# Optimization experiments

Hardware: AMD Instinct MI355X
Metric: run time of the kernel (lower is better)

The kernel has to match this reference:

```python
import jax, jax.numpy as jnp
import numpy as np

USER_NUM = 100000
ITEM_NUM = 50000
N_NODES = USER_NUM + ITEM_NUM
EMB_DIM = 64
N_LAYERS = 3
NNZ = 4800000


def setup_inputs() -> dict:
    key = jax.random.key(0)
    k1, k2, k3, k4, k5 = jax.random.split(key, 5)
    user_emb = 0.2 * jax.random.normal(k1, (USER_NUM, EMB_DIM), dtype=jnp.float32)
    item_emb = 0.2 * jax.random.normal(k2, (ITEM_NUM, EMB_DIM), dtype=jnp.float32)
    adj_row = jax.random.randint(k3, (NNZ,), 0, N_NODES, dtype=jnp.int32)
    adj_col = jax.random.randint(k4, (NNZ,), 0, N_NODES, dtype=jnp.int32)
    adj_vals = jax.random.uniform(k5, (NNZ,), dtype=jnp.float32)
    return {
        "user_emb": user_emb,
        "item_emb": item_emb,
        "adj_row": adj_row,
        "adj_col": adj_col,
        "adj_vals": adj_vals,
    }


def _spmm(row, col, vals, x):
    # sparse [N,N] @ dense [N,D] via gather + weighted segment-sum
    msg = vals[:, None] * x[col]  # [nnz, D]
    return jax.ops.segment_sum(msg, row, num_segments=N_NODES)


def reference(user_emb, item_emb, adj_row, adj_col, adj_vals):
    ego = jnp.concatenate([user_emb, item_emb], axis=0)  # [N, D]
    acc = ego  # running sum over layers (equivalent to stack+mean)
    for _ in range(N_LAYERS):
        ego = _spmm(adj_row, adj_col, adj_vals, ego)
        acc = acc + ego
    out = acc / jnp.asarray(N_LAYERS + 1, dtype=acc.dtype)
    return out[:USER_NUM], out[USER_NUM:]
```

## Files before the change

### kernel.cpp

```cpp
#include <hip/hip_runtime.h>

#define USER_NUM 100000
#define ITEM_NUM 50000
#define N_NODES  150000
#define EMB_DIM  64
#define NNZ      4800000

#define CB_SHIFT 10
#define ROWS_PER_CB 1024
#define NCB ((N_NODES + ROWS_PER_CB - 1) / ROWS_PER_CB)
#define CB_CAP 34000
#define TILE 2048
#define NTILES ((NNZ + TILE - 1) / TILE)
#define EPT 8
#define CUR_STRIDE 16

__device__ __forceinline__ float bflo(unsigned u) {
    return __uint_as_float(u << 16);
}
__device__ __forceinline__ float bfhi(unsigned u) {
    return __uint_as_float(u & 0xFFFF0000u);
}
__device__ __forceinline__ unsigned f2bf(float f) {
    unsigned u = __float_as_uint(f);
    return (u + 0x7FFFu + ((u >> 16) & 1u)) >> 16;
}

__global__ void lgcn_init(const float4* __restrict__ user,
                          const float4* __restrict__ item,
                          uint4* __restrict__ xb,
                          int* __restrict__ bucket_cursor) {
    int i = blockIdx.x * blockDim.x + threadIdx.x;
    if (i < NCB) bucket_cursor[i * CUR_STRIDE] = i * CB_CAP;
    if (i >= N_NODES * 8) return;
    const int user_chunks = USER_NUM * 8;
    float4 f0, f1;
    if (i < user_chunks) {
        f0 = user[i * 2];
        f1 = user[i * 2 + 1];
    } else {
        f0 = item[(i - user_chunks) * 2];
        f1 = item[(i - user_chunks) * 2 + 1];
    }
    uint4 p;
    p.x = f2bf(f0.x) | (f2bf(f0.y) << 16);
    p.y = f2bf(f0.z) | (f2bf(f0.w) << 16);
    p.z = f2bf(f1.x) | (f2bf(f1.y) << 16);
    p.w = f2bf(f1.z) | (f2bf(f1.w) << 16);
    xb[i] = p;
}

__global__ __launch_bounds__(256, 8) void lgcn_partition(
    const int* __restrict__ row,
    const int* __restrict__ col,
    const float* __restrict__ vals,
    int* __restrict__ bucket_cursor,
    int2* __restrict__ t_cv) {
    __shared__ int histB[NCB];
    __shared__ int delta[NCB];
    __shared__ int2 pcv[TILE];
    __shared__ unsigned char bb[TILE];
    int* sscan = (int*)pcv;

    int tid = threadIdx.x;
    int tileStart = blockIdx.x * TILE;
    int tileCount = NNZ - tileStart;
    if (tileCount > TILE) tileCount = TILE;

    for (int b = tid; b < NCB; b += 256) histB[b] = 0;
    __syncthreads();

    int rws[EPT];
    int lps[EPT];
#pragma unroll
    for (int k = 0; k < EPT; ++k) {
        int le = tid + k * 256;
        int r = -1, lp = 0;
        if (le < tileCount) {
            r = row[tileStart + le];
            lp = atomicAdd(&histB[r >> CB_SHIFT], 1);
        }
        rws[k] = r;
        lps[k] = lp;
    }
    __syncthreads();

    int h = (tid < NCB) ? histB[tid] : 0;
    sscan[tid] = h;
    __syncthreads();
    for (int off = 1; off < 256; off <<= 1) {
        int x = (tid >= off) ? sscan[tid - off] : 0;
        __syncthreads();
        sscan[tid] += x;
        __syncthreads();
    }
    int sb = 0, rb = 0;
    if (tid < NCB) {
        sb = sscan[tid] - h;
        rb = h ? atomicAdd(&bucket_cursor[tid * CUR_STRIDE], h) : 0;
    }
    __syncthreads();
    if (tid < NCB) {
        histB[tid] = sb;
        delta[tid] = rb - sb;
    }
    __syncthreads();

#pragma unroll
    for (int k = 0; k < EPT; ++k) {
        int le = tid + k * 256;
        if (le < tileCount) {
            int e = tileStart + le;
            int cc = col[e];
            float vv = vals[e];
            int r = rws[k];
            int b = r >> CB_SHIFT;
            int slot = histB[b] + lps[k];
            pcv[slot] = make_int2(((r & (ROWS_PER_CB - 1)) << 18) | cc,
                                  __float_as_int(vv));
            bb[slot] = (unsigned char)b;
        }
    }
    __syncthreads();

#pragma unroll
    for (int k = 0; k < EPT; ++k) {
        int i = tid + k * 256;
        if (i < tileCount) {
            int b = bb[i];
            int gpos = delta[b] + i;
            if (gpos < (b + 1) * CB_CAP)
                t_cv[gpos] = pcv[i];
        }
    }
}

__global__ __launch_bounds__(1024) void lgcn_finalize(
    const int* __restrict__ bucket_cursor,
    const int2* __restrict__ t_cv,
    int2* __restrict__ csr_cv,
    int2* __restrict__ row_se) {
    __shared__ int hist[ROWS_PER_CB];
    __shared__ int cur[ROWS_PER_CB];
    __shared__ int sscan[1024];
    int t = threadIdx.x;
    int b = blockIdx.x;

    int v = 0;
    if (t < NCB) {
        int cb = bucket_cursor[t * CUR_STRIDE] - t * CB_CAP;
        v = (cb > CB_CAP) ? CB_CAP : cb;
    }
    if (t < 256) sscan[t] = v;
    __syncthreads();
    for (int off = 1; off < 256; off <<= 1) {
        int x = 0;
        if (t < 256 && t >= off) x = sscan[t - off];
        __syncthreads();
        if (t < 256) sscan[t] += x;
        __syncthreads();
    }
    int prev = (b == 0) ? 0 : sscan[b - 1];
    int bbase = prev;
    int count = sscan[b] - prev;
    __syncthreads();

    int lo = b * ROWS_PER_CB;
    int nrows = N_NODES - lo;
    if (nrows > ROWS_PER_CB) nrows = ROWS_PER_CB;

    hist[t] = 0;
    __syncthreads();

    int base = b * CB_CAP;
    int eEnd = base + count;
    int e = base + t;
    for (; e + 3 * 1024 < eEnd; e += 4 * 1024) {
        int2 c0 = t_cv[e];
        int2 c1 = t_cv[e + 1024];
        int2 c2 = t_cv[e + 2048];
        int2 c3 = t_cv[e + 3072];
        atomicAdd(&hist[(unsigned)c0.x >> 18], 1);
        atomicAdd(&hist[(unsigned)c1.x >> 18], 1);
        atomicAdd(&hist[(unsigned)c2.x >> 18], 1);
        atomicAdd(&hist[(unsigned)c3.x >> 18], 1);
    }
    for (; e < eEnd; e += 1024)
        atomicAdd(&hist[(unsigned)t_cv[e].x >> 18], 1);
    __syncthreads();

    int h = hist[t];
    sscan[t] = h;
    __syncthreads();
    for (int off = 1; off < 1024; off <<= 1) {
        int x = (t >= off) ? sscan[t - off] : 0;
        __syncthreads();
        sscan[t] += x;
        __syncthreads();
    }
    int p = bbase + sscan[t] - h;
    if (t < nrows) {
        row_se[lo + t] = make_int2(p, p + h);
        cur[t] = p;
    }
    __syncthreads();

    e = base + t;
    for (; e + 3 * 1024 < eEnd; e += 4 * 1024) {
        int2 c0 = t_cv[e];
        int2 c1 = t_cv[e + 1024];
        int2 c2 = t_cv[e + 2048];
        int2 c3 = t_cv[e + 3072];
        int p0 = atomicAdd(&cur[(unsigned)c0.x >> 18], 1);
        int p1 = atomicAdd(&cur[(unsigned)c1.x >> 18], 1);
        int p2 = atomicAdd(&cur[(unsigned)c2.x >> 18], 1);
        int p3 = atomicAdd(&cur[(unsigned)c3.x >> 18], 1);
        csr_cv[p0] = make_int2(c0.x & 0x3FFFF, c0.y);
        csr_cv[p1] = make_int2(c1.x & 0x3FFFF, c1.y);
        csr_cv[p2] = make_int2(c2.x & 0x3FFFF, c2.y);
        csr_cv[p3] = make_int2(c3.x & 0x3FFFF, c3.y);
    }
    for (; e < eEnd; e += 1024) {
        int2 cv = t_cv[e];
        int pos = atomicAdd(&cur[(unsigned)cv.x >> 18], 1);
        csr_cv[pos] = make_int2(cv.x & 0x3FFFF, cv.y);
    }
}

#define FMA8(vv, uu) do {                                          \
    a[0] += (vv) * bflo((uu).x); a[1] += (vv) * bfhi((uu).x);      \
    a[2] += (vv) * bflo((uu).y); a[3] += (vv) * bfhi((uu).y);      \
    a[4] += (vv) * bflo((uu).z); a[5] += (vv) * bfhi((uu).z);      \
    a[6] += (vv) * bflo((uu).w); a[7] += (vv) * bfhi((uu).w);      \
} while (0)

#define SPMM_BODY                                                  \
    int gid = blockIdx.x * blockDim.x + threadIdx.x;               \
    int r = gid >> 6;                                              \
    if (r >= N_NODES) return;                                      \
    int lane = threadIdx.x & 63;                                   \
    int c = lane & 7;                                              \
    int sub = lane >> 3;                                           \
    int2 se = row_se[r];                                           \
    int start = se.x;                                              \
    int end = se.y;                                                \
    float a[8] = {0.f, 0.f, 0.f, 0.f, 0.f, 0.f, 0.f, 0.f};         \
    int e = start + sub;                                           \
    for (; e + 24 < end; e += 32) {                                \
        int2 cv0 = csr_cv[e];                                      \
        int2 cv1 = csr_cv[e + 8];                                  \
        int2 cv2 = csr_cv[e + 16];                                 \
        int2 cv3 = csr_cv[e + 24];                                 \
        uint4 u0 = xb[cv0.x * 8 + c];                              \
        uint4 u1 = xb[cv1.x * 8 + c];                              \
        uint4 u2 = xb[cv2.x * 8 + c];                              \
        uint4 u3 = xb[cv3.x * 8 + c];                              \
        float v0 = __int_as_float(cv0.y);                          \
        float v1 = __int_as_float(cv1.y);                          \
        float v2 = __int_as_float(cv2.y);                          \
        float v3 = __int_as_float(cv3.y);                          \
        FMA8(v0, u0);                                              \
        FMA8(v1, u1);                                              \
        FMA8(v2, u2);                                              \
        FMA8(v3, u3);                                              \
    }                                                              \
    if (e + 8 < end) {                                             \
        int2 cv0 = csr_cv[e];                                      \
        int2 cv1 = csr_cv[e + 8];                                  \
        uint4 u0 = xb[cv0.x * 8 + c];                              \
        uint4 u1 = xb[cv1.x * 8 + c];                              \
        float v0 = __int_as_float(cv0.y);                          \
        float v1 = __int_as_float(cv1.y);                          \
        FMA8(v0, u0);                                              \
        FMA8(v1, u1);                                              \
        e += 16;                                                   \
    }                                                              \
    if (e < end) {                                                 \
        int2 cv = csr_cv[e];                                       \
        uint4 u = xb[cv.x * 8 + c];                                \
        float v = __int_as_float(cv.y);                            \
        FMA8(v, u);                                                \
    }                                                              \
    _Pragma("unroll")                                              \
    for (int k = 0; k < 8; ++k) {                                  \
        a[k] += __shfl_xor(a[k], 8);                               \
        a[k] += __shfl_xor(a[k], 16);                              \
        a[k] += __shfl_xor(a[k], 32);                              \
    }

__global__ __launch_bounds__(256, 8) void lgcn_spmm_bf16(
    const int2* __restrict__ row_se,
    const int2* __restrict__ csr_cv,
    const uint4* __restrict__ xb,
    uint4* __restrict__ yb) {
    SPMM_BODY
    if (sub == 0) {
        uint4 p;
        p.x = f2bf(a[0]) | (f2bf(a[1]) << 16);
        p.y = f2bf(a[2]) | (f2bf(a[3]) << 16);
        p.z = f2bf(a[4]) | (f2bf(a[5]) << 16);
        p.w = f2bf(a[6]) | (f2bf(a[7]) << 16);
        yb[r * 8 + c] = p;
    }
}

__global__ __launch_bounds__(256, 8) void lgcn_spmm_final(
    const int2* __restrict__ row_se,
    const int2* __restrict__ csr_cv,
    const uint4* __restrict__ xb,
    const uint4* __restrict__ x0b,
    const uint4* __restrict__ y1b,
    float4* __restrict__ out) {
    SPMM_BODY
    if (sub == 0) {
        uint4 q0 = x0b[r * 8 + c];
        uint4 q1 = y1b[r * 8 + c];
        uint4 q2 = xb[r * 8 + c];
        float4 o0, o1;
        o0.x = (bflo(q0.x) + bflo(q1.x) + bflo(q2.x) + a[0]) * 0.25f;
        o0.y = (bfhi(q0.x) + bfhi(q1.x) + bfhi(q2.x) + a[1]) * 0.25f;
        o0.z = (bflo(q0.y) + bflo(q1.y) + bflo(q2.y) + a[2]) * 0.25f;
        o0.w = (bfhi(q0.y) + bfhi(q1.y) + bfhi(q2.y) + a[3]) * 0.25f;
        o1.x = (bflo(q0.z) + bflo(q1.z) + bflo(q2.z) + a[4]) * 0.25f;
        o1.y = (bfhi(q0.z) + bfhi(q1.z) + bfhi(q2.z) + a[5]) * 0.25f;
        o1.z = (bflo(q0.w) + bflo(q1.w) + bflo(q2.w) + a[6]) * 0.25f;
        o1.w = (bfhi(q0.w) + bfhi(q1.w) + bfhi(q2.w) + a[7]) * 0.25f;
        int idx = r * 16 + c * 2;
        out[idx] = o0;
        out[idx + 1] = o1;
    }
}

extern "C" void kernel_launch(void* const* d_in, const int* in_sizes, int n_in,
                              void* d_out, int out_size, void* d_ws, size_t ws_size,
                              hipStream_t stream) {
    const float* user_emb = (const float*)d_in[0];
    const float* item_emb = (const float*)d_in[1];
    const int*   adj_row  = (const int*)d_in[2];
    const int*   adj_col  = (const int*)d_in[3];
    const float* adj_vals = (const float*)d_in[4];
    float* out = (float*)d_out;

    char* base = (char*)d_ws;
    uint4* xb_a   = (uint4*)base;
    int2*  csr_cv = (int2*)(base + 19200000);
    char*  S      = base + 57600000;
    const size_t T_ENTRIES = (size_t)NCB * CB_CAP;
    int2*  t_cv   = (int2*)S;
    uint4* y1b    = (uint4*)S;
    uint4* y2b    = (uint4*)(S + 19200000);
    char*  tail   = S + T_ENTRIES * 8;
    int2*  row_se = (int2*)tail;
    int*   bucket_cursor = (int*)(tail + (size_t)N_NODES * 8);

    {
        int threads = 256;
        int blocks = (N_NODES * 8 + threads - 1) / threads;
        lgcn_init<<<blocks, threads, 0, stream>>>(
            (const float4*)user_emb, (const float4*)item_emb, xb_a,
            bucket_cursor);
    }

    lgcn_partition<<<NTILES, 256, 0, stream>>>(
        adj_row, adj_col, adj_vals, bucket_cursor, t_cv);
    lgcn_finalize<<<NCB, 1024, 0, stream>>>(
        bucket_cursor, t_cv, csr_cv, row_se);

    const int spmm_block = 256;
    const int spmm_grid = (N_NODES * 64 + spmm_block - 1) / spmm_block;
    lgcn_spmm_bf16<<<spmm_grid, spmm_block, 0, stream>>>(
        row_se, csr_cv, xb_a, y1b);
    lgcn_spmm_bf16<<<spmm_grid, spmm_block, 0, stream>>>(
        row_se, csr_cv, y1b, y2b);
    lgcn_spmm_final<<<spmm_grid, spmm_block, 0, stream>>>(
        row_se, csr_cv, y2b, xb_a, y1b, (float4*)out);
}
```

Measured before the change: 507.9 us.

## Halve row buckets, widen partition blocks, use nontemporal loads/stores in SpMM

Row buckets shrink from 1024 to 512 rows, which doubles the bucket count to 293. The partition kernel moves to 512 threads per block so its scan covers every bucket, and the finalize scan widens to 1024 entries. The SpMM kernels switch the CSR edge stream, the layer outputs and the final output to nontemporal loads and stores, so the gathered embedding rows keep more of the cache. The trade-off is more global cursor atomics and per-block scan work during partitioning, in exchange for smaller finalize blocks and less cache pollution.

```diff
diff --git a/kernel.cpp b/kernel.cpp
--- a/kernel.cpp
+++ b/kernel.cpp
@@ -6,13 +6,14 @@
 #define EMB_DIM  64
 #define NNZ      4800000
 
-#define CB_SHIFT 10
-#define ROWS_PER_CB 1024
+#define CB_SHIFT 9
+#define ROWS_PER_CB 512
 #define NCB ((N_NODES + ROWS_PER_CB - 1) / ROWS_PER_CB)
-#define CB_CAP 34000
+#define CB_CAP 17024
 #define TILE 2048
 #define NTILES ((NNZ + TILE - 1) / TILE)
-#define EPT 8
+#define PT_THREADS 512
+#define EPT (TILE / PT_THREADS)
 #define CUR_STRIDE 16
 
 __device__ __forceinline__ float bflo(unsigned u) {
@@ -24,6 +25,27 @@
 __device__ __forceinline__ unsigned f2bf(float f) {
     unsigned u = __float_as_uint(f);
     return (u + 0x7FFFu + ((u >> 16) & 1u)) >> 16;
+}
+
+typedef int      evi2 __attribute__((ext_vector_type(2)));
+typedef unsigned evu4 __attribute__((ext_vector_type(4)));
+typedef float    evf4 __attribute__((ext_vector_type(4)));
+
+__device__ __forceinline__ int2 ntload_i2(const int2* p) {
+    evi2 t = __builtin_nontemporal_load((const evi2*)p);
+    return make_int2(t.x, t.y);
+}
+__device__ __forceinline__ uint4 ntload_u4(const uint4* p) {
+    evu4 t = __builtin_nontemporal_load((const evu4*)p);
+    uint4 r; r.x = t.x; r.y = t.y; r.z = t.z; r.w = t.w; return r;
+}
+__device__ __forceinline__ void ntstore_u4(uint4* p, uint4 v) {
+    evu4 t; t.x = v.x; t.y = v.y; t.z = v.z; t.w = v.w;
+    __builtin_nontemporal_store(t, (evu4*)p);
+}
+__device__ __forceinline__ void ntstore_f4(float4* p, float4 v) {
+    evf4 t; t.x = v.x; t.y = v.y; t.z = v.z; t.w = v.w;
+    __builtin_nontemporal_store(t, (evf4*)p);
 }
 
 __global__ void lgcn_init(const float4* __restrict__ user,
@@ -50,7 +72,7 @@
     xb[i] = p;
 }
 
-__global__ __launch_bounds__(256, 8) void lgcn_partition(
+__global__ __launch_bounds__(PT_THREADS, 8) void lgcn_partition(
     const int* __restrict__ row,
     const int* __restrict__ col,
     const float* __restrict__ vals,
@@ -59,7 +81,7 @@
     __shared__ int histB[NCB];
     __shared__ int delta[NCB];
     __shared__ int2 pcv[TILE];
-    __shared__ unsigned char bb[TILE];
+    __shared__ unsigned short bb[TILE];
     int* sscan = (int*)pcv;
 
     int tid = threadIdx.x;
@@ -67,14 +89,14 @@
     int tileCount = NNZ - tileStart;
     if (tileCount > TILE) tileCount = TILE;
 
-    for (int b = tid; b < NCB; b += 256) histB[b] = 0;
+    for (int b = tid; b < NCB; b += PT_THREADS) histB[b] = 0;
     __syncthreads();
 
     int rws[EPT];
     int lps[EPT];
 #pragma unroll
     for (int k = 0; k < EPT; ++k) {
-        int le = tid + k * 256;
+        int le = tid + k * PT_THREADS;
         int r = -1, lp = 0;
         if (le < tileCount) {
             r = row[tileStart + le];
@@ -88,7 +110,7 @@
     int h = (tid < NCB) ? histB[tid] : 0;
     sscan[tid] = h;
     __syncthreads();
-    for (int off = 1; off < 256; off <<= 1) {
+    for (int off = 1; off < PT_THREADS; off <<= 1) {
         int x = (tid >= off) ? sscan[tid - off] : 0;
         __syncthreads();
         sscan[tid] += x;
@@ -108,7 +130,7 @@
 
 #pragma unroll
     for (int k = 0; k < EPT; ++k) {
-        int le = tid + k * 256;
+        int le = tid + k * PT_THREADS;
         if (le < tileCount) {
             int e = tileStart + le;
             int cc = col[e];
@@ -118,14 +140,14 @@
             int slot = histB[b] + lps[k];
             pcv[slot] = make_int2(((r & (ROWS_PER_CB - 1)) << 18) | cc,
                                   __float_as_int(vv));
-            bb[slot] = (unsigned char)b;
+            bb[slot] = (unsigned short)b;
         }
     }
     __syncthreads();
 
 #pragma unroll
     for (int k = 0; k < EPT; ++k) {
-        int i = tid + k * 256;
+        int i = tid + k * PT_THREADS;
         if (i < tileCount) {
             int b = bb[i];
             int gpos = delta[b] + i;
@@ -151,25 +173,23 @@
         int cb = bucket_cursor[t * CUR_STRIDE] - t * CB_CAP;
         v = (cb > CB_CAP) ? CB_CAP : cb;
     }
-    if (t < 256) sscan[t] = v;
-    __syncthreads();
-    for (int off = 1; off < 256; off <<= 1) {
-        int x = 0;
-        if (t < 256 && t >= off) x = sscan[t - off];
-        __syncthreads();
-        if (t < 256) sscan[t] += x;
+    sscan[t] = v;
+    __syncthreads();
+    for (int off = 1; off < 1024; off <<= 1) {
+        int x = (t >= off) ? sscan[t - off] : 0;
+        __syncthreads();
+        sscan[t] += x;
         __syncthreads();
     }
     int prev = (b == 0) ? 0 : sscan[b - 1];
     int bbase = prev;
     int count = sscan[b] - prev;
-    __syncthreads();
 
     int lo = b * ROWS_PER_CB;
     int nrows = N_NODES - lo;
     if (nrows > ROWS_PER_CB) nrows = ROWS_PER_CB;
 
-    hist[t] = 0;
+    if (t < ROWS_PER_CB) hist[t] = 0;
     __syncthreads();
 
     int base = b * CB_CAP;
@@ -189,7 +209,7 @@
         atomicAdd(&hist[(unsigned)t_cv[e].x >> 18], 1);
     __syncthreads();
 
-    int h = hist[t];
+    int h = (t < ROWS_PER_CB) ? hist[t] : 0;
     sscan[t] = h;
     __syncthreads();
     for (int off = 1; off < 1024; off <<= 1) {
@@ -247,10 +267,10 @@
     float a[8] = {0.f, 0.f, 0.f, 0.f, 0.f, 0.f, 0.f, 0.f};         \
     int e = start + sub;                                           \
     for (; e + 24 < end; e += 32) {                                \
-        int2 cv0 = csr_cv[e];                                      \
-        int2 cv1 = csr_cv[e + 8];                                  \
-        int2 cv2 = csr_cv[e + 16];                                 \
-        int2 cv3 = csr_cv[e + 24];                                 \
+        int2 cv0 = ntload_i2(&csr_cv[e]);                          \
+        int2 cv1 = ntload_i2(&csr_cv[e + 8]);                      \
+        int2 cv2 = ntload_i2(&csr_cv[e + 16]);                     \
+        int2 cv3 = ntload_i2(&csr_cv[e + 24]);                     \
         uint4 u0 = xb[cv0.x * 8 + c];                              \
         uint4 u1 = xb[cv1.x * 8 + c];                              \
         uint4 u2 = xb[cv2.x * 8 + c];                              \
@@ -265,8 +285,8 @@
         FMA8(v3, u3);                                              \
     }                                                              \
     if (e + 8 < end) {                                             \
-        int2 cv0 = csr_cv[e];                                      \
-        int2 cv1 = csr_cv[e + 8];                                  \
+        int2 cv0 = ntload_i2(&csr_cv[e]);                          \
+        int2 cv1 = ntload_i2(&csr_cv[e + 8]);                      \
         uint4 u0 = xb[cv0.x * 8 + c];                              \
         uint4 u1 = xb[cv1.x * 8 + c];                              \
         float v0 = __int_as_float(cv0.y);                          \
@@ -276,7 +296,7 @@
         e += 16;                                                   \
     }                                                              \
     if (e < end) {                                                 \
-        int2 cv = csr_cv[e];                                       \
+        int2 cv = ntload_i2(&csr_cv[e]);                           \
         uint4 u = xb[cv.x * 8 + c];                                \
         float v = __int_as_float(cv.y);                            \
         FMA8(v, u);                                                \
@@ -300,7 +320,7 @@
         p.y = f2bf(a[2]) | (f2bf(a[3]) << 16);
         p.z = f2bf(a[4]) | (f2bf(a[5]) << 16);
         p.w = f2bf(a[6]) | (f2bf(a[7]) << 16);
-        yb[r * 8 + c] = p;
+        ntstore_u4(&yb[r * 8 + c], p);
     }
 }
 
@@ -313,8 +333,8 @@
     float4* __restrict__ out) {
     SPMM_BODY
     if (sub == 0) {
-        uint4 q0 = x0b[r * 8 + c];
-        uint4 q1 = y1b[r * 8 + c];
+        uint4 q0 = ntload_u4(&x0b[r * 8 + c]);
+        uint4 q1 = ntload_u4(&y1b[r * 8 + c]);
         uint4 q2 = xb[r * 8 + c];
         float4 o0, o1;
         o0.x = (bflo(q0.x) + bflo(q1.x) + bflo(q2.x) + a[0]) * 0.25f;
@@ -326,8 +346,8 @@
         o1.z = (bflo(q0.w) + bflo(q1.w) + bflo(q2.w) + a[6]) * 0.25f;
         o1.w = (bfhi(q0.w) + bfhi(q1.w) + bfhi(q2.w) + a[7]) * 0.25f;
         int idx = r * 16 + c * 2;
-        out[idx] = o0;
-        out[idx + 1] = o1;
+        ntstore_f4(&out[idx], o0);
+        ntstore_f4(&out[idx + 1], o1);
     }
 }
 
@@ -361,7 +381,7 @@
             bucket_cursor);
     }
 
-    lgcn_partition<<<NTILES, 256, 0, stream>>>(
+    lgcn_partition<<<NTILES, PT_THREADS, 0, stream>>>(
         adj_row, adj_col, adj_vals, bucket_cursor, t_cv);
     lgcn_finalize<<<NCB, 1024, 0, stream>>>(
         bucket_cursor, t_cv, csr_cv, row_se);
```

Measured after the change: 532.5 us. 4.9% more time.
